# Kernel optimization log

Hardware: AMD Instinct MI355X
Metric: run time of the kernel (lower is better)

Reference implementation:

```python
import jax, jax.numpy as jnp
import numpy as np

B, NV, NRINGS, NDIRS, C, F = 2, 20000, 8, 8, 16, 16


def setup_inputs() -> dict:
    key = jax.random.key(0)
    ks = jax.random.split(key, 7)
    y = jax.random.normal(ks[0], (B, NV, NDIRS, C), jnp.float32)
    contributors = jax.random.randint(ks[1], (NV, NRINGS, NDIRS, 3), 0, NV, dtype=jnp.int32)
    weights_bary = jax.random.uniform(ks[2], (NV, NRINGS, NDIRS, 3), jnp.float32)
    angles = jax.random.randint(ks[3], (NV, NRINGS, NDIRS, 3), 0, NDIRS, dtype=jnp.int32)
    kernel = jax.random.normal(ks[4], (NRINGS, NDIRS, C, F), jnp.float32) * 0.05
    center_kernel = jax.random.normal(ks[5], (C, F), jnp.float32) * 0.05
    bias = jnp.zeros((F,), jnp.float32)
    return {"y": y, "contributors": contributors, "weights_bary": weights_bary,
            "angles": angles, "kernel": kernel, "center_kernel": center_kernel, "bias": bias}


def reference(y, contributors, weights_bary, angles, kernel, center_kernel, bias):
    # y: (B, nv, ndirs, C); tables: (nv, nrings, ndirs, 3)
    b, nv, ndirs, nch = y.shape
    nfilters = kernel.shape[-1]
    nrings = contributors.shape[1]

    # window_interpolation_sync: gather 3 contributor vertices per window bin,
    # with the direction axis re-indexed per-contributor (radial sync), then
    # barycentric-weighted sum.  Flatten (vertex, dir) into one gather index.
    idx = contributors * ndirs + angles                 # (nv, nrings, ndirs, 3)
    y_flat = y.reshape(b, nv * ndirs, nch)
    gathered = y_flat[:, idx, :]                        # (B, nv, nrings, ndirs, 3, C)
    z = jnp.einsum('bvrdjc,vrdj->bvrdc', gathered, weights_bary)  # (B, nv, nrings, ndirs, C)

    # gcnn_conv: circular pad over dirs then VALID conv with (nrings, ndirs) kernel
    zr = z.reshape(b * nv, nrings, ndirs, nch)
    zr = jnp.concatenate([zr, zr[:, :, :-1, :]], axis=2)  # width 2*ndirs-1
    conv = jax.lax.conv_general_dilated(
        zr, kernel, window_strides=(1, 1), padding='VALID',
        dimension_numbers=('NHWC', 'HWIO', 'NHWC'))       # (B*nv, 1, ndirs, F)
    conv = conv.reshape(b, nv, ndirs, nfilters)

    out = conv + jnp.einsum('bvdc,cf->bvdf', y, center_kernel) + bias
    out = jax.nn.relu(out)
    return jnp.max(out, axis=2)                          # take_max over directions -> (B, nv, F)
```

## Files before the change

kernel.cpp:

```cpp
#include <hip/hip_runtime.h>

typedef unsigned short u16;
typedef __attribute__((ext_vector_type(4))) unsigned int u32x4;
typedef __attribute__((ext_vector_type(4))) float f32x4;
typedef __attribute__((ext_vector_type(8))) __bf16 bf16x8;

constexpr int BATCH = 2;
constexpr int NV    = 20000;
constexpr int ND    = 8;
constexpr int CH    = 16;
constexpr int NF    = 16;
constexpr int NVD   = NV * ND;
constexpr int K0    = 1024;
constexpr int KE    = 1152;
constexpr int NCHUNK = KE / 32;
constexpr int MTOT  = BATCH * NV;
constexpr int BSTR  = 40;

constexpr size_t Y16_OFF_B = 0;
constexpr size_t K2C_OFF_B = 10240000;
constexpr size_t ZC_OFF_B  = 10534912;

__device__ __forceinline__ u16 f2bf(float x) {
    unsigned int u = __float_as_uint(x);
    unsigned int r = (u + 0x7fffu + ((u >> 16) & 1u)) >> 16;
    return (u16)r;
}
__device__ __forceinline__ unsigned int pack2bf(float a, float b) {
    return (unsigned int)f2bf(a) | ((unsigned int)f2bf(b) << 16);
}

__global__ __launch_bounds__(256) void prep(const float* __restrict__ y,
                                            u16* __restrict__ y16,
                                            u16* __restrict__ zc) {
    int tid = blockIdx.x * 256 + threadIdx.x;
    const float4* src = (const float4*)(y + (size_t)tid * 16);
    float4 v0 = src[0], v1 = src[1], v2 = src[2], v3 = src[3];
    u32x4 lo = {pack2bf(v0.x, v0.y), pack2bf(v0.z, v0.w), pack2bf(v1.x, v1.y), pack2bf(v1.z, v1.w)};
    u32x4 hi = {pack2bf(v2.x, v2.y), pack2bf(v2.z, v2.w), pack2bf(v3.x, v3.y), pack2bf(v3.z, v3.w)};
    u16* yd = y16 + (size_t)tid * 16;
    *(u32x4*)(yd)     = lo;
    *(u32x4*)(yd + 8) = hi;
    int iv = tid >> 3, d = tid & 7;
    u16* zd = zc + ((size_t)(32 + (d >> 1)) * MTOT + iv) * 32 + (d & 1) * 16;
    *(u32x4*)(zd)     = lo;
    *(u32x4*)(zd + 8) = hi;
}

__global__ __launch_bounds__(256) void k2_build(const float* __restrict__ kern,
                                                const float* __restrict__ ck,
                                                u16* __restrict__ k2c) {
    int e = blockIdx.x * 256 + threadIdx.x;
    int i = e & 4095;
    int kc = e >> 12;
    int n = i >> 5, kk = i & 31;
    int k = kc * 32 + kk;
    int w = n >> 4, f = n & 15;
    float val;
    if (k < K0) {
        int r = k >> 7, dd = (k >> 4) & 7, c = k & 15;
        int d = (dd - w) & 7;
        val = kern[((r * 8 + d) * 16 + c) * 16 + f];
    } else {
        int ke = k - K0;
        int d = ke >> 4, c = ke & 15;
        val = (d == w) ? ck[c * 16 + f] : 0.f;
    }
    k2c[e] = f2bf(val);
}

__global__ __launch_bounds__(256) void gather(const u16* __restrict__ y16,
                                              const int* __restrict__ contrib,
                                              const float* __restrict__ wbary,
                                              const int* __restrict__ angles,
                                              u16* __restrict__ zc) {
    int item = blockIdx.x * 256 + threadIdx.x;
    int iv = item >> 6, rd = item & 63;
    int b = iv >= NV;
    int v = iv - b * NV;
    size_t mb = ((size_t)v * 64 + rd) * 3;
    const u16* ybase = y16 + (size_t)b * NVD * CH;

    float acc[CH];
    #pragma unroll
    for (int c = 0; c < CH; ++c) acc[c] = 0.f;
    #pragma unroll
    for (int j = 0; j < 3; ++j) {
        int cn = contrib[mb + j];
        int an = angles[mb + j];
        float wj = wbary[mb + j];
        const u16* src = ybase + ((size_t)cn * ND + an) * CH;
        u32x4 p0 = *(const u32x4*)(src);
        u32x4 p1 = *(const u32x4*)(src + 8);
        #pragma unroll
        for (int q = 0; q < 4; ++q) {
            unsigned int u = p0[q];
            acc[2 * q]     += wj * __uint_as_float(u << 16);
            acc[2 * q + 1] += wj * __uint_as_float(u & 0xffff0000u);
        }
        #pragma unroll
        for (int q = 0; q < 4; ++q) {
            unsigned int u = p1[q];
            acc[8 + 2 * q]     += wj * __uint_as_float(u << 16);
            acc[8 + 2 * q + 1] += wj * __uint_as_float(u & 0xffff0000u);
        }
    }
    u32x4 o0, o1;
    #pragma unroll
    for (int q = 0; q < 4; ++q) {
        o0[q] = pack2bf(acc[2 * q], acc[2 * q + 1]);
        o1[q] = pack2bf(acc[8 + 2 * q], acc[8 + 2 * q + 1]);
    }
    u16* dst = zc + ((size_t)(rd >> 1) * MTOT + iv) * 32 + (rd & 1) * 16;
    *(u32x4*)(dst)     = o0;
    *(u32x4*)(dst + 8) = o1;
}

__global__ __launch_bounds__(256) void gemm_max(const u16* __restrict__ zc,
                                                const u16* __restrict__ k2c,
                                                const float* __restrict__ bias,
                                                float* __restrict__ out) {
    __shared__ __align__(16) u16 Bb[2][128 * BSTR];
    const int t = threadIdx.x;
    const int w = t >> 6, lane = t & 63;
    const int lrow = lane & 15, lq = lane >> 4;
    const int m0 = blockIdx.x * 64;
    const int arow = m0 + w * 16 + lrow;

    const int sn = t >> 1, sh = (t & 1) * 16;

    {
        const u32x4* src = (const u32x4*)(k2c + (size_t)0 * 4096 + sn * 32 + sh);
        u32x4 b0 = src[0], b1 = src[1];
        u16* dst = &Bb[0][sn * BSTR + sh];
        *(u32x4*)(dst)     = b0;
        *(u32x4*)(dst + 8) = b1;
    }
    bf16x8 a_next = *(const bf16x8*)(zc + ((size_t)0 * MTOT + arow) * 32 + lq * 8);

    f32x4 acc[8];
    #pragma unroll
    for (int nt = 0; nt < 8; ++nt) acc[nt] = (f32x4){0.f, 0.f, 0.f, 0.f};

    for (int kc = 0; kc < NCHUNK; ++kc) {
        __syncthreads();
        bf16x8 a = a_next;
        u32x4 bn0, bn1;
        if (kc < NCHUNK - 1) {
            a_next = *(const bf16x8*)(zc + ((size_t)(kc + 1) * MTOT + arow) * 32 + lq * 8);
            const u32x4* src = (const u32x4*)(k2c + (size_t)(kc + 1) * 4096 + sn * 32 + sh);
            bn0 = src[0]; bn1 = src[1];
        }
        bf16x8 bf[8];
        #pragma unroll
        for (int nt = 0; nt < 8; ++nt)
            bf[nt] = *(const bf16x8*)(&Bb[kc & 1][(nt * 16 + lrow) * BSTR + lq * 8]);
        #pragma unroll
        for (int nt = 0; nt < 8; ++nt)
            acc[nt] = __builtin_amdgcn_mfma_f32_16x16x32_bf16(a, bf[nt], acc[nt], 0, 0, 0);
        if (kc < NCHUNK - 1) {
            u16* dst = &Bb[(kc + 1) & 1][sn * BSTR + sh];
            *(u32x4*)(dst)     = bn0;
            *(u32x4*)(dst + 8) = bn1;
        }
    }

    const float bb = bias[lrow];
    #pragma unroll
    for (int reg = 0; reg < 4; ++reg) {
        float m = 0.f;
        #pragma unroll
        for (int nt = 0; nt < 8; ++nt) m = fmaxf(m, acc[nt][reg] + bb);
        out[((size_t)(m0 + w * 16 + lq * 4 + reg)) * NF + lrow] = m;
    }
}

extern "C" void kernel_launch(void* const* d_in, const int* in_sizes, int n_in,
                              void* d_out, int out_size, void* d_ws, size_t ws_size,
                              hipStream_t stream) {
    const float* y      = (const float*)d_in[0];
    const int*   contrib= (const int*)d_in[1];
    const float* wbary  = (const float*)d_in[2];
    const int*   angles = (const int*)d_in[3];
    const float* kern   = (const float*)d_in[4];
    const float* ck     = (const float*)d_in[5];
    const float* bias   = (const float*)d_in[6];
    float* out = (float*)d_out;

    u16* y16 = (u16*)((char*)d_ws + Y16_OFF_B);
    u16* k2c = (u16*)((char*)d_ws + K2C_OFF_B);
    u16* zc  = (u16*)((char*)d_ws + ZC_OFF_B);

    prep<<<1250, 256, 0, stream>>>(y, y16, zc);
    k2_build<<<(NCHUNK * 4096) / 256, 256, 0, stream>>>(kern, ck, k2c);
    gather<<<10000, 256, 0, stream>>>(y16, contrib, wbary, angles, zc);
    gemm_max<<<MTOT / 64, 256, 0, stream>>>(zc, k2c, bias, out);
}
```

Measured before the change: 216.8 us.

## Interleave batches in bf16 y copy so gather serves both batches per index

The bf16 copy of y is laid out so both batch entries of each (vertex, direction) sit next to each other. Each gather thread then loads the contributor, angle and weight tables once and fetches 64 contiguous bytes covering both batches, which halves index-table traffic and the number of gather threads. The index-table loads are also marked nontemporal. The GEMM kernel prefetches A fragments two chunks ahead instead of one. The cost is more registers per gather thread, with two accumulator sets, and one extra A register set in the GEMM.

After: 236.9 us. +9.2%, slower.

```diff
diff --git a/kernel.cpp b/kernel.cpp
--- a/kernel.cpp
+++ b/kernel.cpp
@@ -10,7 +10,6 @@
 constexpr int ND    = 8;
 constexpr int CH    = 16;
 constexpr int NF    = 16;
-constexpr int NVD   = NV * ND;
 constexpr int K0    = 1024;
 constexpr int KE    = 1152;
 constexpr int NCHUNK = KE / 32;
@@ -31,17 +30,20 @@
 }
 
 __global__ __launch_bounds__(256) void prep(const float* __restrict__ y,
-                                            u16* __restrict__ y16,
+                                            u16* __restrict__ y16i,
                                             u16* __restrict__ zc) {
     int tid = blockIdx.x * 256 + threadIdx.x;
+    int b = tid >= 160000;
+    int vd = tid - b * 160000;
     const float4* src = (const float4*)(y + (size_t)tid * 16);
     float4 v0 = src[0], v1 = src[1], v2 = src[2], v3 = src[3];
     u32x4 lo = {pack2bf(v0.x, v0.y), pack2bf(v0.z, v0.w), pack2bf(v1.x, v1.y), pack2bf(v1.z, v1.w)};
     u32x4 hi = {pack2bf(v2.x, v2.y), pack2bf(v2.z, v2.w), pack2bf(v3.x, v3.y), pack2bf(v3.z, v3.w)};
-    u16* yd = y16 + (size_t)tid * 16;
+    u16* yd = y16i + ((size_t)vd * 2 + b) * 16;
     *(u32x4*)(yd)     = lo;
     *(u32x4*)(yd + 8) = hi;
-    int iv = tid >> 3, d = tid & 7;
+    int v = vd >> 3, d = vd & 7;
+    int iv = b * NV + v;
     u16* zd = zc + ((size_t)(32 + (d >> 1)) * MTOT + iv) * 32 + (d & 1) * 16;
     *(u32x4*)(zd)     = lo;
     *(u32x4*)(zd + 8) = hi;
@@ -69,51 +71,66 @@
     k2c[e] = f2bf(val);
 }
 
-__global__ __launch_bounds__(256) void gather(const u16* __restrict__ y16,
+__global__ __launch_bounds__(256) void gather(const u16* __restrict__ y16i,
                                               const int* __restrict__ contrib,
                                               const float* __restrict__ wbary,
                                               const int* __restrict__ angles,
                                               u16* __restrict__ zc) {
     int item = blockIdx.x * 256 + threadIdx.x;
-    int iv = item >> 6, rd = item & 63;
-    int b = iv >= NV;
-    int v = iv - b * NV;
+    int v = item >> 6, rd = item & 63;
     size_t mb = ((size_t)v * 64 + rd) * 3;
-    const u16* ybase = y16 + (size_t)b * NVD * CH;
-
-    float acc[CH];
-    #pragma unroll
-    for (int c = 0; c < CH; ++c) acc[c] = 0.f;
+
+    float a0[CH], a1[CH];
+    #pragma unroll
+    for (int c = 0; c < CH; ++c) { a0[c] = 0.f; a1[c] = 0.f; }
     #pragma unroll
     for (int j = 0; j < 3; ++j) {
-        int cn = contrib[mb + j];
-        int an = angles[mb + j];
-        float wj = wbary[mb + j];
-        const u16* src = ybase + ((size_t)cn * ND + an) * CH;
-        u32x4 p0 = *(const u32x4*)(src);
-        u32x4 p1 = *(const u32x4*)(src + 8);
+        int cn   = __builtin_nontemporal_load(contrib + mb + j);
+        int an   = __builtin_nontemporal_load(angles + mb + j);
+        float wj = __builtin_nontemporal_load(wbary + mb + j);
+        const u32x4* src = (const u32x4*)(y16i + ((size_t)(cn * ND + an)) * 32);
+        u32x4 p0 = src[0], p1 = src[1];
+        u32x4 p2 = src[2], p3 = src[3];
         #pragma unroll
         for (int q = 0; q < 4; ++q) {
             unsigned int u = p0[q];
-            acc[2 * q]     += wj * __uint_as_float(u << 16);
-            acc[2 * q + 1] += wj * __uint_as_float(u & 0xffff0000u);
+            a0[2 * q]     += wj * __uint_as_float(u << 16);
+            a0[2 * q + 1] += wj * __uint_as_float(u & 0xffff0000u);
         }
         #pragma unroll
         for (int q = 0; q < 4; ++q) {
             unsigned int u = p1[q];
-            acc[8 + 2 * q]     += wj * __uint_as_float(u << 16);
-            acc[8 + 2 * q + 1] += wj * __uint_as_float(u & 0xffff0000u);
-        }
-    }
-    u32x4 o0, o1;
+            a0[8 + 2 * q]     += wj * __uint_as_float(u << 16);
+            a0[8 + 2 * q + 1] += wj * __uint_as_float(u & 0xffff0000u);
+        }
+        #pragma unroll
+        for (int q = 0; q < 4; ++q) {
+            unsigned int u = p2[q];
+            a1[2 * q]     += wj * __uint_as_float(u << 16);
+            a1[2 * q + 1] += wj * __uint_as_float(u & 0xffff0000u);
+        }
+        #pragma unroll
+        for (int q = 0; q < 4; ++q) {
+            unsigned int u = p3[q];
+            a1[8 + 2 * q]     += wj * __uint_as_float(u << 16);
+            a1[8 + 2 * q + 1] += wj * __uint_as_float(u & 0xffff0000u);
+        }
+    }
+    u32x4 o0, o1, o2, o3;
     #pragma unroll
     for (int q = 0; q < 4; ++q) {
-        o0[q] = pack2bf(acc[2 * q], acc[2 * q + 1]);
-        o1[q] = pack2bf(acc[8 + 2 * q], acc[8 + 2 * q + 1]);
-    }
-    u16* dst = zc + ((size_t)(rd >> 1) * MTOT + iv) * 32 + (rd & 1) * 16;
-    *(u32x4*)(dst)     = o0;
-    *(u32x4*)(dst + 8) = o1;
+        o0[q] = pack2bf(a0[2 * q], a0[2 * q + 1]);
+        o1[q] = pack2bf(a0[8 + 2 * q], a0[8 + 2 * q + 1]);
+        o2[q] = pack2bf(a1[2 * q], a1[2 * q + 1]);
+        o3[q] = pack2bf(a1[8 + 2 * q], a1[8 + 2 * q + 1]);
+    }
+    size_t zoff = ((size_t)(rd >> 1) * MTOT) * 32 + (size_t)(rd & 1) * 16;
+    u16* d0 = zc + zoff + (size_t)v * 32;
+    u16* d1 = zc + zoff + (size_t)(v + NV) * 32;
+    *(u32x4*)(d0)     = o0;
+    *(u32x4*)(d0 + 8) = o1;
+    *(u32x4*)(d1)     = o2;
+    *(u32x4*)(d1 + 8) = o3;
 }
 
 __global__ __launch_bounds__(256) void gemm_max(const u16* __restrict__ zc,
@@ -126,17 +143,19 @@
     const int lrow = lane & 15, lq = lane >> 4;
     const int m0 = blockIdx.x * 64;
     const int arow = m0 + w * 16 + lrow;
+    const u16* abase = zc + (size_t)arow * 32 + lq * 8;
 
     const int sn = t >> 1, sh = (t & 1) * 16;
 
     {
-        const u32x4* src = (const u32x4*)(k2c + (size_t)0 * 4096 + sn * 32 + sh);
+        const u32x4* src = (const u32x4*)(k2c + (size_t)sn * 32 + sh);
         u32x4 b0 = src[0], b1 = src[1];
         u16* dst = &Bb[0][sn * BSTR + sh];
         *(u32x4*)(dst)     = b0;
         *(u32x4*)(dst + 8) = b1;
     }
-    bf16x8 a_next = *(const bf16x8*)(zc + ((size_t)0 * MTOT + arow) * 32 + lq * 8);
+    bf16x8 a_p0 = *(const bf16x8*)(abase);
+    bf16x8 a_p1 = *(const bf16x8*)(abase + (size_t)1 * MTOT * 32);
 
     f32x4 acc[8];
     #pragma unroll
@@ -144,10 +163,12 @@
 
     for (int kc = 0; kc < NCHUNK; ++kc) {
         __syncthreads();
-        bf16x8 a = a_next;
+        bf16x8 a = a_p0;
+        a_p0 = a_p1;
+        if (kc < NCHUNK - 2)
+            a_p1 = *(const bf16x8*)(abase + (size_t)(kc + 2) * MTOT * 32);
         u32x4 bn0, bn1;
         if (kc < NCHUNK - 1) {
-            a_next = *(const bf16x8*)(zc + ((size_t)(kc + 1) * MTOT + arow) * 32 + lq * 8);
             const u32x4* src = (const u32x4*)(k2c + (size_t)(kc + 1) * 4096 + sn * 32 + sh);
             bn0 = src[0]; bn1 = src[1];
         }
@@ -187,12 +208,12 @@
     const float* bias   = (const float*)d_in[6];
     float* out = (float*)d_out;
 
-    u16* y16 = (u16*)((char*)d_ws + Y16_OFF_B);
-    u16* k2c = (u16*)((char*)d_ws + K2C_OFF_B);
-    u16* zc  = (u16*)((char*)d_ws + ZC_OFF_B);
-
-    prep<<<1250, 256, 0, stream>>>(y, y16, zc);
+    u16* y16i = (u16*)((char*)d_ws + Y16_OFF_B);
+    u16* k2c  = (u16*)((char*)d_ws + K2C_OFF_B);
+    u16* zc   = (u16*)((char*)d_ws + ZC_OFF_B);
+
+    prep<<<1250, 256, 0, stream>>>(y, y16i, zc);
     k2_build<<<(NCHUNK * 4096) / 256, 256, 0, stream>>>(kern, ck, k2c);
-    gather<<<10000, 256, 0, stream>>>(y16, contrib, wbary, angles, zc);
+    gather<<<5000, 256, 0, stream>>>(y16i, contrib, wbary, angles, zc);
     gemm_max<<<MTOT / 64, 256, 0, stream>>>(zc, k2c, bias, out);
 }
```

## Fuse gather into MFMA GEMM via shared-memory staging, merge prep kernels

Applied to the files above, without the earlier changes.

Fuses the barycentric gather into the GEMM+max kernel. Each block interpolates a 32-vertex tile of A chunks straight into double-buffered LDS, so the bf16 intermediate z is never written to or read back from global memory. The two setup kernels are merged into one launch, and the GEMM is split per batch into two launches. Per-wave output tiling changes to 2x2 with an LDS atomicMax reduction across the column waves. The cost is more work per K-step and a gather latency that sits on the GEMM's critical path.

New measurement: 265.6 us. +22.5%, slower.

```diff
diff --git a/kernel.cpp b/kernel.cpp
--- a/kernel.cpp
+++ b/kernel.cpp
@@ -12,14 +12,12 @@
 constexpr int NF    = 16;
 constexpr int NVD   = NV * ND;
 constexpr int K0    = 1024;
-constexpr int KE    = 1152;
-constexpr int NCHUNK = KE / 32;
-constexpr int MTOT  = BATCH * NV;
+constexpr int NCHUNK = 36;
+constexpr int MV    = 32;
+constexpr int ZSTR  = 40;
 constexpr int BSTR  = 40;
 
-constexpr size_t Y16_OFF_B = 0;
 constexpr size_t K2C_OFF_B = 10240000;
-constexpr size_t ZC_OFF_B  = 10534912;
 
 __device__ __forceinline__ u16 f2bf(float x) {
     unsigned int u = __float_as_uint(x);
@@ -30,149 +28,181 @@
     return (unsigned int)f2bf(a) | ((unsigned int)f2bf(b) << 16);
 }
 
-__global__ __launch_bounds__(256) void prep(const float* __restrict__ y,
-                                            u16* __restrict__ y16,
-                                            u16* __restrict__ zc) {
-    int tid = blockIdx.x * 256 + threadIdx.x;
-    const float4* src = (const float4*)(y + (size_t)tid * 16);
-    float4 v0 = src[0], v1 = src[1], v2 = src[2], v3 = src[3];
-    u32x4 lo = {pack2bf(v0.x, v0.y), pack2bf(v0.z, v0.w), pack2bf(v1.x, v1.y), pack2bf(v1.z, v1.w)};
-    u32x4 hi = {pack2bf(v2.x, v2.y), pack2bf(v2.z, v2.w), pack2bf(v3.x, v3.y), pack2bf(v3.z, v3.w)};
-    u16* yd = y16 + (size_t)tid * 16;
-    *(u32x4*)(yd)     = lo;
-    *(u32x4*)(yd + 8) = hi;
-    int iv = tid >> 3, d = tid & 7;
-    u16* zd = zc + ((size_t)(32 + (d >> 1)) * MTOT + iv) * 32 + (d & 1) * 16;
-    *(u32x4*)(zd)     = lo;
-    *(u32x4*)(zd + 8) = hi;
-}
-
-__global__ __launch_bounds__(256) void k2_build(const float* __restrict__ kern,
-                                                const float* __restrict__ ck,
-                                                u16* __restrict__ k2c) {
-    int e = blockIdx.x * 256 + threadIdx.x;
-    int i = e & 4095;
-    int kc = e >> 12;
-    int n = i >> 5, kk = i & 31;
-    int k = kc * 32 + kk;
-    int w = n >> 4, f = n & 15;
-    float val;
-    if (k < K0) {
-        int r = k >> 7, dd = (k >> 4) & 7, c = k & 15;
-        int d = (dd - w) & 7;
-        val = kern[((r * 8 + d) * 16 + c) * 16 + f];
+__global__ __launch_bounds__(256) void prep_k2(const float* __restrict__ y,
+                                               const float* __restrict__ kern,
+                                               const float* __restrict__ ck,
+                                               u16* __restrict__ y16,
+                                               u16* __restrict__ k2c) {
+    int bx = blockIdx.x;
+    if (bx < 1250) {
+        int tid = bx * 256 + threadIdx.x;
+        const float4* src = (const float4*)(y + (size_t)tid * 16);
+        float4 v0 = src[0], v1 = src[1], v2 = src[2], v3 = src[3];
+        u32x4 lo = {pack2bf(v0.x, v0.y), pack2bf(v0.z, v0.w), pack2bf(v1.x, v1.y), pack2bf(v1.z, v1.w)};
+        u32x4 hi = {pack2bf(v2.x, v2.y), pack2bf(v2.z, v2.w), pack2bf(v3.x, v3.y), pack2bf(v3.z, v3.w)};
+        u16* yd = y16 + (size_t)tid * 16;
+        *(u32x4*)(yd)     = lo;
+        *(u32x4*)(yd + 8) = hi;
     } else {
-        int ke = k - K0;
-        int d = ke >> 4, c = ke & 15;
-        val = (d == w) ? ck[c * 16 + f] : 0.f;
-    }
-    k2c[e] = f2bf(val);
-}
-
-__global__ __launch_bounds__(256) void gather(const u16* __restrict__ y16,
-                                              const int* __restrict__ contrib,
-                                              const float* __restrict__ wbary,
-                                              const int* __restrict__ angles,
-                                              u16* __restrict__ zc) {
-    int item = blockIdx.x * 256 + threadIdx.x;
-    int iv = item >> 6, rd = item & 63;
-    int b = iv >= NV;
-    int v = iv - b * NV;
-    size_t mb = ((size_t)v * 64 + rd) * 3;
-    const u16* ybase = y16 + (size_t)b * NVD * CH;
-
-    float acc[CH];
+        int e = (bx - 1250) * 256 + threadIdx.x;
+        int i = e & 4095, kc = e >> 12;
+        int n = i >> 5, kk = i & 31;
+        int k = kc * 32 + kk;
+        int w = n >> 4, f = n & 15;
+        float val;
+        if (k < K0) {
+            int r = k >> 7, dd = (k >> 4) & 7, c = k & 15;
+            int d = (dd - w) & 7;
+            val = kern[((r * 8 + d) * 16 + c) * 16 + f];
+        } else {
+            int ke = k - K0;
+            int d = ke >> 4, c = ke & 15;
+            val = (d == w) ? ck[c * 16 + f] : 0.f;
+        }
+        k2c[e] = f2bf(val);
+    }
+}
+
+struct Meta { int c0, c1, c2, a0, a1, a2; float w0, w1, w2; };
+
+__global__ __launch_bounds__(256, 4) void geo_fused(const u16* __restrict__ y16b,
+                                                    const u16* __restrict__ k2c,
+                                                    const int* __restrict__ contrib,
+                                                    const float* __restrict__ wbary,
+                                                    const int* __restrict__ angles,
+                                                    const float* __restrict__ bias,
+                                                    float* __restrict__ outb) {
+    __shared__ __align__(16) u16 Zb[2][MV * ZSTR];
+    __shared__ __align__(16) u16 Bb[2][128 * BSTR];
+
+    const int t = threadIdx.x;
+    const int v0 = blockIdx.x * MV;
+    const int vl = t >> 3, rdo = (t >> 2) & 1, q = t & 3;
+    const int sn = t >> 1, sh = (t & 1) * 16;
+    const int wid = t >> 6, lane = t & 63;
+    const int wr = wid & 1, wc = wid >> 1;
+    const int lrow = lane & 15, lq = lane >> 4;
+
+    const size_t mrow = (size_t)(v0 + vl) * 64;
+
+#define LOAD_META(M, j)                                                            \
+    {   size_t mb = (mrow + ((j) * 2 + rdo)) * 3;                                  \
+        (M).c0 = __builtin_nontemporal_load(contrib + mb);                         \
+        (M).c1 = __builtin_nontemporal_load(contrib + mb + 1);                     \
+        (M).c2 = __builtin_nontemporal_load(contrib + mb + 2);                     \
+        (M).a0 = __builtin_nontemporal_load(angles + mb);                          \
+        (M).a1 = __builtin_nontemporal_load(angles + mb + 1);                      \
+        (M).a2 = __builtin_nontemporal_load(angles + mb + 2);                      \
+        (M).w0 = __builtin_nontemporal_load(wbary + mb);                           \
+        (M).w1 = __builtin_nontemporal_load(wbary + mb + 1);                       \
+        (M).w2 = __builtin_nontemporal_load(wbary + mb + 2); }
+
+#define ISSUE_GATHER(M, g0, g1, g2)                                                \
+    {   g0 = *(const uint2*)(y16b + ((size_t)((M).c0 * 8 + (M).a0)) * 16 + q * 4); \
+        g1 = *(const uint2*)(y16b + ((size_t)((M).c1 * 8 + (M).a1)) * 16 + q * 4); \
+        g2 = *(const uint2*)(y16b + ((size_t)((M).c2 * 8 + (M).a2)) * 16 + q * 4); }
+
+#define COMBINE_WRITE(M, g0, g1, g2, buf)                                          \
+    {   float x0 = 0.f, x1 = 0.f, x2 = 0.f, x3 = 0.f;                              \
+        x0 += (M).w0 * __uint_as_float(g0.x << 16);                                \
+        x1 += (M).w0 * __uint_as_float(g0.x & 0xffff0000u);                        \
+        x2 += (M).w0 * __uint_as_float(g0.y << 16);                                \
+        x3 += (M).w0 * __uint_as_float(g0.y & 0xffff0000u);                        \
+        x0 += (M).w1 * __uint_as_float(g1.x << 16);                                \
+        x1 += (M).w1 * __uint_as_float(g1.x & 0xffff0000u);                        \
+        x2 += (M).w1 * __uint_as_float(g1.y << 16);                                \
+        x3 += (M).w1 * __uint_as_float(g1.y & 0xffff0000u);                        \
+        x0 += (M).w2 * __uint_as_float(g2.x << 16);                                \
+        x1 += (M).w2 * __uint_as_float(g2.x & 0xffff0000u);                        \
+        x2 += (M).w2 * __uint_as_float(g2.y << 16);                                \
+        x3 += (M).w2 * __uint_as_float(g2.y & 0xffff0000u);                        \
+        uint2 o; o.x = pack2bf(x0, x1); o.y = pack2bf(x2, x3);                     \
+        *(uint2*)(&Zb[buf][vl * ZSTR + rdo * 16 + q * 4]) = o; }
+
+#define STAGE_B(kcn, b0v, b1v)                                                     \
+    {   const u32x4* src = (const u32x4*)(k2c + (size_t)(kcn) * 4096 + sn * 32 + sh); \
+        b0v = src[0]; b1v = src[1]; }
+
+#define WRITE_B(buf, b0v, b1v)                                                     \
+    {   u16* dst = &Bb[buf][sn * BSTR + sh];                                       \
+        *(u32x4*)(dst) = b0v; *(u32x4*)(dst + 8) = b1v; }
+
+#define CENTER_LOAD(kcn, g0)                                                       \
+    {   g0 = *(const uint2*)(y16b + ((size_t)((v0 + vl) * 8 + ((kcn) - 32) * 2 + rdo)) * 16 + q * 4); }
+
+    Meta M;
+    uint2 g0, g1, g2;
+    u32x4 b0v, b1v;
+    LOAD_META(M, 0);
+    ISSUE_GATHER(M, g0, g1, g2);
+    STAGE_B(0, b0v, b1v);
+    Meta Mn;
+    LOAD_META(Mn, 1);
+    COMBINE_WRITE(M, g0, g1, g2, 0);
+    WRITE_B(0, b0v, b1v);
+    M = Mn;
+    __syncthreads();
+
+    f32x4 acc[4];
     #pragma unroll
-    for (int c = 0; c < CH; ++c) acc[c] = 0.f;
-    #pragma unroll
-    for (int j = 0; j < 3; ++j) {
-        int cn = contrib[mb + j];
-        int an = angles[mb + j];
-        float wj = wbary[mb + j];
-        const u16* src = ybase + ((size_t)cn * ND + an) * CH;
-        u32x4 p0 = *(const u32x4*)(src);
-        u32x4 p1 = *(const u32x4*)(src + 8);
+    for (int j = 0; j < 4; ++j) acc[j] = (f32x4){0.f, 0.f, 0.f, 0.f};
+
+    for (int kc = 0; kc < NCHUNK; ++kc) {
+        const int p = kc & 1;
+        const int kcn = kc + 1;
+        const bool more = kcn < NCHUNK;
+        const bool rnd  = kcn < 32;
+
+        if (more) {
+            if (rnd) { ISSUE_GATHER(M, g0, g1, g2); }
+            else     { CENTER_LOAD(kcn, g0); }
+            STAGE_B(kcn, b0v, b1v);
+            if (kcn + 1 < 32) { LOAD_META(Mn, kcn + 1); }
+        }
+
+        bf16x8 af = *(const bf16x8*)(&Zb[p][(wr * 16 + lrow) * ZSTR + lq * 8]);
+        bf16x8 bf[4];
         #pragma unroll
-        for (int q = 0; q < 4; ++q) {
-            unsigned int u = p0[q];
-            acc[2 * q]     += wj * __uint_as_float(u << 16);
-            acc[2 * q + 1] += wj * __uint_as_float(u & 0xffff0000u);
+        for (int j = 0; j < 4; ++j)
+            bf[j] = *(const bf16x8*)(&Bb[p][((wc * 4 + j) * 16 + lrow) * BSTR + lq * 8]);
+        #pragma unroll
+        for (int j = 0; j < 4; ++j)
+            acc[j] = __builtin_amdgcn_mfma_f32_16x16x32_bf16(af, bf[j], acc[j], 0, 0, 0);
+
+        if (more) {
+            const int wb = kcn & 1;
+            if (rnd) { COMBINE_WRITE(M, g0, g1, g2, wb); M = Mn; }
+            else {
+                *(uint2*)(&Zb[wb][vl * ZSTR + rdo * 16 + q * 4]) = g0;
+            }
+            WRITE_B(wb, b0v, b1v);
         }
-        #pragma unroll
-        for (int q = 0; q < 4; ++q) {
-            unsigned int u = p1[q];
-            acc[8 + 2 * q]     += wj * __uint_as_float(u << 16);
-            acc[8 + 2 * q + 1] += wj * __uint_as_float(u & 0xffff0000u);
-        }
-    }
-    u32x4 o0, o1;
-    #pragma unroll
-    for (int q = 0; q < 4; ++q) {
-        o0[q] = pack2bf(acc[2 * q], acc[2 * q + 1]);
-        o1[q] = pack2bf(acc[8 + 2 * q], acc[8 + 2 * q + 1]);
-    }
-    u16* dst = zc + ((size_t)(rd >> 1) * MTOT + iv) * 32 + (rd & 1) * 16;
-    *(u32x4*)(dst)     = o0;
-    *(u32x4*)(dst + 8) = o1;
-}
-
-__global__ __launch_bounds__(256) void gemm_max(const u16* __restrict__ zc,
-                                                const u16* __restrict__ k2c,
-                                                const float* __restrict__ bias,
-                                                float* __restrict__ out) {
-    __shared__ __align__(16) u16 Bb[2][128 * BSTR];
-    const int t = threadIdx.x;
-    const int w = t >> 6, lane = t & 63;
-    const int lrow = lane & 15, lq = lane >> 4;
-    const int m0 = blockIdx.x * 64;
-    const int arow = m0 + w * 16 + lrow;
-
-    const int sn = t >> 1, sh = (t & 1) * 16;
-
-    {
-        const u32x4* src = (const u32x4*)(k2c + (size_t)0 * 4096 + sn * 32 + sh);
-        u32x4 b0 = src[0], b1 = src[1];
-        u16* dst = &Bb[0][sn * BSTR + sh];
-        *(u32x4*)(dst)     = b0;
-        *(u32x4*)(dst + 8) = b1;
-    }
-    bf16x8 a_next = *(const bf16x8*)(zc + ((size_t)0 * MTOT + arow) * 32 + lq * 8);
-
-    f32x4 acc[8];
-    #pragma unroll
-    for (int nt = 0; nt < 8; ++nt) acc[nt] = (f32x4){0.f, 0.f, 0.f, 0.f};
-
-    for (int kc = 0; kc < NCHUNK; ++kc) {
         __syncthreads();
-        bf16x8 a = a_next;
-        u32x4 bn0, bn1;
-        if (kc < NCHUNK - 1) {
-            a_next = *(const bf16x8*)(zc + ((size_t)(kc + 1) * MTOT + arow) * 32 + lq * 8);
-            const u32x4* src = (const u32x4*)(k2c + (size_t)(kc + 1) * 4096 + sn * 32 + sh);
-            bn0 = src[0]; bn1 = src[1];
-        }
-        bf16x8 bf[8];
-        #pragma unroll
-        for (int nt = 0; nt < 8; ++nt)
-            bf[nt] = *(const bf16x8*)(&Bb[kc & 1][(nt * 16 + lrow) * BSTR + lq * 8]);
-        #pragma unroll
-        for (int nt = 0; nt < 8; ++nt)
-            acc[nt] = __builtin_amdgcn_mfma_f32_16x16x32_bf16(a, bf[nt], acc[nt], 0, 0, 0);
-        if (kc < NCHUNK - 1) {
-            u16* dst = &Bb[(kc + 1) & 1][sn * BSTR + sh];
-            *(u32x4*)(dst)     = bn0;
-            *(u32x4*)(dst + 8) = bn1;
-        }
-    }
-
+    }
+
+    int* emax = (int*)&Bb[0][0];
+    for (int e = t; e < MV * NF; e += 256) emax[e] = 0;
+    __syncthreads();
     const float bb = bias[lrow];
     #pragma unroll
     for (int reg = 0; reg < 4; ++reg) {
         float m = 0.f;
         #pragma unroll
-        for (int nt = 0; nt < 8; ++nt) m = fmaxf(m, acc[nt][reg] + bb);
-        out[((size_t)(m0 + w * 16 + lq * 4 + reg)) * NF + lrow] = m;
-    }
+        for (int j = 0; j < 4; ++j) m = fmaxf(m, acc[j][reg] + bb);
+        int row = wr * 16 + lq * 4 + reg;
+        atomicMax(&emax[row * NF + lrow], __float_as_int(m));
+    }
+    __syncthreads();
+    for (int e = t; e < MV * NF; e += 256) {
+        int row = e >> 4, f = e & 15;
+        __builtin_nontemporal_store(__int_as_float(emax[e]), outb + (size_t)(v0 + row) * NF + f);
+    }
+#undef LOAD_META
+#undef ISSUE_GATHER
+#undef COMBINE_WRITE
+#undef STAGE_B
+#undef WRITE_B
+#undef CENTER_LOAD
 }
 
 extern "C" void kernel_launch(void* const* d_in, const int* in_sizes, int n_in,
@@ -187,12 +217,11 @@
     const float* bias   = (const float*)d_in[6];
     float* out = (float*)d_out;
 
-    u16* y16 = (u16*)((char*)d_ws + Y16_OFF_B);
+    u16* y16 = (u16*)d_ws;
     u16* k2c = (u16*)((char*)d_ws + K2C_OFF_B);
-    u16* zc  = (u16*)((char*)d_ws + ZC_OFF_B);
-
-    prep<<<1250, 256, 0, stream>>>(y, y16, zc);
-    k2_build<<<(NCHUNK * 4096) / 256, 256, 0, stream>>>(kern, ck, k2c);
-    gather<<<10000, 256, 0, stream>>>(y16, contrib, wbary, angles, zc);
-    gemm_max<<<MTOT / 64, 256, 0, stream>>>(zc, k2c, bias, out);
-}
+
+    prep_k2<<<1250 + 576, 256, 0, stream>>>(y, kern, ck, y16, k2c);
+    geo_fused<<<NV / MV, 256, 0, stream>>>(y16, k2c, contrib, wbary, angles, bias, out);
+    geo_fused<<<NV / MV, 256, 0, stream>>>(y16 + (size_t)NVD * CH, k2c, contrib, wbary, angles,
+                                           bias, out + (size_t)NV * NF);
+}
```
